# Kernel optimization log

Measured on AMD Instinct MI355X. Metric: run time of the kernel, lower is better.

Reference implementation:

```python
import jax, jax.numpy as jnp
import numpy as np

HIDDEN = 64
NUM_LAYERS = 6
BN_EPS = 1e-5


def setup_inputs() -> dict:
    key = jax.random.key(0)
    N, M = 1024, 1024
    num_nodes = N + M
    ks = jax.random.split(key, 12)
    x = jax.random.normal(ks[0], (num_nodes, 2), dtype=jnp.float32)
    # complete bipartite edges: (a, N+b) for all a in [0,N), b in [0,M), row-major so view(N,M) is meaningful
    row = jnp.repeat(jnp.arange(N, dtype=jnp.int64), M)
    col = N + jnp.tile(jnp.arange(M, dtype=jnp.int64), N)
    edge_index = jnp.stack([row, col], axis=0)
    s = 1.0 / np.sqrt(HIDDEN)
    return {
        "x": x,
        "edge_index": edge_index,
        "in_w": jax.random.normal(ks[1], (2, HIDDEN), jnp.float32) * 0.5,
        "in_b": jnp.zeros((HIDDEN,), jnp.float32),
        "conv_w": jax.random.normal(ks[2], (NUM_LAYERS, HIDDEN, HIDDEN), jnp.float32) * s,
        "conv_b": jnp.zeros((NUM_LAYERS, HIDDEN), jnp.float32),
        "bn_gamma": jnp.ones((NUM_LAYERS, HIDDEN), jnp.float32),
        "bn_beta": jnp.zeros((NUM_LAYERS, HIDDEN), jnp.float32),
        "out_w": jax.random.normal(ks[3], (2 * HIDDEN, 1), jnp.float32) * s,
        "out_b": jnp.zeros((1,), jnp.float32),
        "N": N,
        "M": M,
    }


def reference(x, edge_index, in_w, in_b, conv_w, conv_b, bn_gamma, bn_beta, out_w, out_b, N, M):
    num_nodes = x.shape[0]
    # GCN normalization with added self-loops (PyG GCNConv defaults)
    loops = jnp.arange(num_nodes, dtype=edge_index.dtype)
    row = jnp.concatenate([edge_index[0], loops])
    col = jnp.concatenate([edge_index[1], loops])
    deg = jax.ops.segment_sum(jnp.ones_like(col, dtype=x.dtype), col, num_segments=num_nodes)
    dinv = jnp.where(deg > 0, jax.lax.rsqrt(deg), 0.0)
    norm = dinv[row] * dinv[col]  # [E+num_nodes]

    h = jax.nn.relu(x @ in_w + in_b)
    for i in range(NUM_LAYERS):
        h_res = h
        hw = h @ conv_w[i]
        agg = jax.ops.segment_sum(hw[row] * norm[:, None], col, num_segments=num_nodes)
        h = agg + conv_b[i]
        # BatchNorm1d in training mode: batch stats, biased variance
        mu = h.mean(axis=0)
        var = ((h - mu) ** 2).mean(axis=0)
        h = (h - mu) * jax.lax.rsqrt(var + BN_EPS) * bn_gamma[i] + bn_beta[i]
        h = jax.nn.relu(h)
        if i > 0 and i % 2 == 1:
            h = h + h_res

    ef = jnp.concatenate([h[edge_index[0]], h[edge_index[1]]], axis=1)  # [E, 2H]
    scores = (ef @ out_w + out_b)[:, 0]
    return scores.reshape(N, M)
```

## Files before the change

kernel.cpp:

```cpp
#include <hip/hip_runtime.h>


#define NBLK 64
#define TAG_BASE 0x5EED1A00u

__device__ __forceinline__ float relu_(float x) { return x > 0.f ? x : 0.f; }

#define AT_LOAD(p)    __hip_atomic_load((p), __ATOMIC_RELAXED, __HIP_MEMORY_SCOPE_AGENT)
#define AT_STORE(p,v) __hip_atomic_store((p), (v), __ATOMIC_RELAXED, __HIP_MEMORY_SCOPE_AGENT)

#define ST_STRIDE_ULL 8192
#define UV_OFF        98304

__device__ __forceinline__ float2 poll_slots(const unsigned long long* stL,
                                             int slot0, int lane, unsigned tagexp)
{
    const unsigned long long* base = stL + lane * 2;
    for (;;) {
        unsigned long long sv[16], qv[16];
#pragma unroll
        for (int j = 0; j < 16; j++) {
            const unsigned long long* p = base + (slot0 + j) * 128;
            sv[j] = AT_LOAD(p);
            qv[j] = AT_LOAD(p + 1);
        }
        bool ok = true;
#pragma unroll
        for (int j = 0; j < 16; j++)
            ok = ok && ((unsigned)(sv[j] >> 32) == tagexp)
                    && ((unsigned)(qv[j] >> 32) == tagexp);
        if (ok) {
            float S = 0.f, Q = 0.f;
#pragma unroll
            for (int j = 0; j < 16; j++) {
                S += __uint_as_float((unsigned)sv[j]);
                Q += __uint_as_float((unsigned)qv[j]);
            }
            return make_float2(S, Q);
        }
        __builtin_amdgcn_s_sleep(1);
    }
}

__global__ __launch_bounds__(256, 1) void k_fused(
    const float* __restrict__ x,
    const float* __restrict__ in_w, const float* __restrict__ in_b,
    const float* __restrict__ conv_w,
    const float* __restrict__ bn_g, const float* __restrict__ bn_b,
    const float* __restrict__ out_w,
    unsigned int* __restrict__ ws)
{
    __shared__ float Wl[2][4096];
    __shared__ float hl[2048];
    __shared__ float Pp[3 * 2048];
    __shared__ float2 pstat[4][64];
    __shared__ float pcoef[64], scoef[64];
    __shared__ float g_lds[384], b_lds[384];
    __shared__ float ow_lds[128];

    const int t = threadIdx.x, b = blockIdx.x;
    const int w    = t >> 6;
    const int lane = t & 63;
    const int fi   = lane & 7;
    const int f0   = fi * 8;
    const int ng   = lane >> 3;
    const int n0   = ng * 4;
    const int sw   = ng & 3;
    const int kb   = w * 16;
    const bool isA = b < 32;
    unsigned long long* stu = (unsigned long long*)ws;
    float* uv = (float*)ws + UV_OFF;

    {
        const float4* src = (const float4*)conv_w;
        float4* dst = (float4*)Wl[0];
        dst[t]       = src[t];
        dst[t + 256] = src[t + 256];
        dst[t + 512] = src[t + 512];
        dst[t + 768] = src[t + 768];
        for (int i = t; i < 384; i += 256) { g_lds[i] = bn_g[i]; b_lds[i] = bn_b[i]; }
        if (t < 128) ow_lds[t] = out_w[t];
    }

    {
        const int nl = t >> 3, fj = (t & 7) * 8;
        const int rsw = (nl >> 2) & 3;
        const int node = b * 32 + nl;
        float x0 = x[node * 2], x1 = x[node * 2 + 1];
#pragma unroll
        for (int j = 0; j < 8; j++) {
            int f = fj + j;
            float v = relu_(fmaf(x0, in_w[f], fmaf(x1, in_w[64 + f], in_b[f])));
            hl[nl * 64 + ((((f >> 2)) ^ rsw) << 2) + (f & 3)] = v;
        }
    }
    __syncthreads();

    for (int layer = 0; layer < 6; layer++) {
        const float* Wb = Wl[layer & 1];
        float acc[4][8];
#pragma unroll
        for (int n = 0; n < 4; n++)
#pragma unroll
            for (int j = 0; j < 8; j++) acc[n][j] = 0.f;

#pragma unroll
        for (int kk = 0; kk < 16; kk += 4) {
            const int cb = (kb + kk) >> 2;
            float hv[4][4];
#pragma unroll
            for (int n = 0; n < 4; n++) {
                float4 h4 = *(const float4*)&hl[(n0 + n) * 64 + ((cb ^ sw) << 2)];
                hv[n][0] = h4.x; hv[n][1] = h4.y; hv[n][2] = h4.z; hv[n][3] = h4.w;
            }
#pragma unroll
            for (int j = 0; j < 4; j++) {
                const float* wr = Wb + (kb + kk + j) * 64 + f0;
                float4 w0 = *(const float4*)wr;
                float4 w1 = *(const float4*)(wr + 4);
                float wv[8] = {w0.x, w0.y, w0.z, w0.w, w1.x, w1.y, w1.z, w1.w};
#pragma unroll
                for (int n = 0; n < 4; n++)
#pragma unroll
                    for (int q = 0; q < 8; q++)
                        acc[n][q] = fmaf(hv[n][j], wv[q], acc[n][q]);
            }
        }

        float4 pf[6];
        const int idx = (w - 1) * 64 + lane;
        if (w > 0) {
            if (layer < 5) {
                const float4* src = (const float4*)(conv_w + (layer + 1) * 4096);
#pragma unroll
                for (int r = 0; r < 5; r++) pf[r] = src[idx + 192 * r];
                if (idx < 64) pf[5] = src[idx + 960];
            }
            float* Pw = Pp + (w - 1) * 2048;
#pragma unroll
            for (int n = 0; n < 4; n++) {
                float* prow = Pw + (n0 + n) * 64;
                *(float4*)&prow[((2 * fi)     ^ sw) << 2] =
                    make_float4(acc[n][0], acc[n][1], acc[n][2], acc[n][3]);
                *(float4*)&prow[((2 * fi + 1) ^ sw) << 2] =
                    make_float4(acc[n][4], acc[n][5], acc[n][6], acc[n][7]);
            }
        }
        __syncthreads();

        const unsigned tagexp = TAG_BASE + (unsigned)layer;
        unsigned long long* stL = stu + layer * ST_STRIDE_ULL;

        if (w == 0) {
#pragma unroll
            for (int r = 0; r < 3; r++) {
                const float* Pr = Pp + r * 2048;
#pragma unroll
                for (int n = 0; n < 4; n++) {
                    const float* prow = Pr + (n0 + n) * 64;
                    float4 p0 = *(const float4*)&prow[((2 * fi)     ^ sw) << 2];
                    float4 p1 = *(const float4*)&prow[((2 * fi + 1) ^ sw) << 2];
                    acc[n][0] += p0.x; acc[n][1] += p0.y; acc[n][2] += p0.z; acc[n][3] += p0.w;
                    acc[n][4] += p1.x; acc[n][5] += p1.y; acc[n][6] += p1.z; acc[n][7] += p1.w;
                }
            }
            float sv[8], qv[8];
#pragma unroll
            for (int j = 0; j < 8; j++) {
                sv[j] = (acc[0][j] + acc[1][j]) + (acc[2][j] + acc[3][j]);
                qv[j] = fmaf(acc[0][j], acc[0][j], fmaf(acc[1][j], acc[1][j],
                        fmaf(acc[2][j], acc[2][j], acc[3][j] * acc[3][j])));
            }
#pragma unroll
            for (int m = 8; m < 64; m <<= 1) {
#pragma unroll
                for (int j = 0; j < 8; j++) {
                    sv[j] += __shfl_xor(sv[j], m);
                    qv[j] += __shfl_xor(qv[j], m);
                }
            }
            {
                unsigned long long spack = ((unsigned long long)tagexp << 32)
                                         | (unsigned long long)__float_as_uint(sv[ng]);
                unsigned long long qpack = ((unsigned long long)tagexp << 32)
                                         | (unsigned long long)__float_as_uint(qv[ng]);
                unsigned long long* p = stL + b * 128 + (fi * 8 + ng) * 2;
                AT_STORE(p, spack);
                AT_STORE(p + 1, qpack);
            }
        }

        {
            float2 myp = poll_slots(stL, w * 16, lane, tagexp);
            pstat[w][lane] = myp;
        }
        __syncthreads();

        if (w > 0) {
            if (layer < 5) {
                float4* dst = (float4*)Wl[(layer + 1) & 1];
#pragma unroll
                for (int r = 0; r < 5; r++) dst[idx + 192 * r] = pf[r];
                if (idx < 64) dst[idx + 960] = pf[5];
            }
        } else {
            float2 a0 = pstat[0][lane], a1 = pstat[1][lane];
            float2 b0 = pstat[2][lane], b1 = pstat[3][lane];
            float SA = a0.x + a1.x, QA = a0.y + a1.y;
            float SB = b0.x + b1.x, QB = b0.y + b1.y;
            {
                const float c1 = 9.75609756097561e-4f;
                const float c2 = 3.1234752377721214e-2f;
                float sumAgg = SA + c1 * SB + 1024.f * c2 * SA;
                float sumSq  = QA + c1 * c1 * QB + 2.f * c1 * c2 * SA * SB
                             + 1024.f * c2 * c2 * SA * SA;
                float meanAgg = sumAgg * (1.f / 2048.f);
                float var = sumSq * (1.f / 2048.f) - meanAgg * meanAgg;
                float rstd = rsqrtf(var + 1e-5f);
                float scale = rstd * g_lds[layer * 64 + lane];
                float bt = b_lds[layer * 64 + lane];
                if (isA) { pcoef[lane] = scale;      scoef[lane] = bt - meanAgg * scale; }
                else     { pcoef[lane] = c1 * scale; scoef[lane] = bt + (c2 * SA - meanAgg) * scale; }
            }
            float pc[8], sc[8];
            {
                float4 p0 = *(const float4*)&pcoef[f0];
                float4 p1 = *(const float4*)&pcoef[f0 + 4];
                float4 s0 = *(const float4*)&scoef[f0];
                float4 s1 = *(const float4*)&scoef[f0 + 4];
                pc[0] = p0.x; pc[1] = p0.y; pc[2] = p0.z; pc[3] = p0.w;
                pc[4] = p1.x; pc[5] = p1.y; pc[6] = p1.z; pc[7] = p1.w;
                sc[0] = s0.x; sc[1] = s0.y; sc[2] = s0.z; sc[3] = s0.w;
                sc[4] = s1.x; sc[5] = s1.y; sc[6] = s1.z; sc[7] = s1.w;
            }

            float vals[4][8];
#pragma unroll
            for (int n = 0; n < 4; n++)
#pragma unroll
                for (int j = 0; j < 8; j++)
                    vals[n][j] = relu_(fmaf(acc[n][j], pc[j], sc[j]));
            if (layer == 1 || layer == 3 || layer == 5) {
#pragma unroll
                for (int n = 0; n < 4; n++) {
                    const float* hrow = hl + (n0 + n) * 64;
                    float4 r0 = *(const float4*)&hrow[((2 * fi)     ^ sw) << 2];
                    float4 r1 = *(const float4*)&hrow[((2 * fi + 1) ^ sw) << 2];
                    vals[n][0] += r0.x; vals[n][1] += r0.y; vals[n][2] += r0.z; vals[n][3] += r0.w;
                    vals[n][4] += r1.x; vals[n][5] += r1.y; vals[n][6] += r1.z; vals[n][7] += r1.w;
                }
            }
            if (layer < 5) {
#pragma unroll
                for (int n = 0; n < 4; n++) {
                    float* hrow = hl + (n0 + n) * 64;
                    *(float4*)&hrow[((2 * fi)     ^ sw) << 2] =
                        make_float4(vals[n][0], vals[n][1], vals[n][2], vals[n][3]);
                    *(float4*)&hrow[((2 * fi + 1) ^ sw) << 2] =
                        make_float4(vals[n][4], vals[n][5], vals[n][6], vals[n][7]);
                }
            } else {
                const float* wv = ow_lds + (isA ? 0 : 64) + f0;
                float4 o0 = *(const float4*)wv;
                float4 o1 = *(const float4*)(wv + 4);
                float d[4];
#pragma unroll
                for (int n = 0; n < 4; n++) {
                    d[n] = fmaf(vals[n][0], o0.x, fmaf(vals[n][1], o0.y,
                           fmaf(vals[n][2], o0.z, fmaf(vals[n][3], o0.w,
                           fmaf(vals[n][4], o1.x, fmaf(vals[n][5], o1.y,
                           fmaf(vals[n][6], o1.z, vals[n][7] * o1.w)))))));
                    d[n] += __shfl_xor(d[n], 1);
                    d[n] += __shfl_xor(d[n], 2);
                    d[n] += __shfl_xor(d[n], 4);
                }
                if (fi == 0) {
#pragma unroll
                    for (int n = 0; n < 4; n++)
                        AT_STORE((unsigned*)(uv + b * 32 + n0 + n),
                                 __float_as_uint(d[n]));
                }
            }
        }
        __syncthreads();
    }
}

__global__ __launch_bounds__(256) void k_out(const float* __restrict__ uv,
                                             const float* __restrict__ out_b,
                                             float* __restrict__ out) {
    const int a = blockIdx.x;
    const int t = threadIdx.x;
    float ua = uv[a] + out_b[0];
    float4 vv = ((const float4*)(uv + 1024))[t];
    ((float4*)(out + a * 1024))[t] =
        make_float4(ua + vv.x, ua + vv.y, ua + vv.z, ua + vv.w);
}

extern "C" void kernel_launch(void* const* d_in, const int* in_sizes, int n_in,
                              void* d_out, int out_size, void* d_ws, size_t ws_size,
                              hipStream_t stream) {
    const float* x      = (const float*)d_in[0];
    const float* in_w   = (const float*)d_in[2];
    const float* in_b   = (const float*)d_in[3];
    const float* conv_w = (const float*)d_in[4];
    const float* bn_g   = (const float*)d_in[6];
    const float* bn_b   = (const float*)d_in[7];
    const float* out_w  = (const float*)d_in[8];
    const float* out_b  = (const float*)d_in[9];
    float* out = (float*)d_out;

    unsigned int* ws = (unsigned int*)d_ws;
    const float* uv = (const float*)ws + UV_OFF;

    k_fused<<<NBLK, 256, 0, stream>>>(x, in_w, in_b, conv_w, bn_g, bn_b,
                                      out_w, ws);
    k_out<<<1024, 256, 0, stream>>>(uv, out_b, out);
}
```

Measured before the change: 116.2 us.

## Fuse output broadcast into persistent kernel using tagged flag-polled u/v values

Removes the separate k_out launch. Each block now publishes its per-node output projection as a tagged 64-bit word, then polls until all u/v values carry the tag and writes 16 rows of the N×M score matrix itself. This saves a kernel launch and its gap at the cost of a grid-wide spin wait at the end of the fused kernel. Only 64 blocks do the output write instead of 1024, which may reduce write bandwidth.

```diff
diff --git a/kernel.cpp b/kernel.cpp
--- a/kernel.cpp
+++ b/kernel.cpp
@@ -3,6 +3,7 @@
 
 #define NBLK 64
 #define TAG_BASE 0x5EED1A00u
+#define TAG_UV   (TAG_BASE + 6u)
 
 __device__ __forceinline__ float relu_(float x) { return x > 0.f ? x : 0.f; }
 
@@ -10,7 +11,7 @@
 #define AT_STORE(p,v) __hip_atomic_store((p), (v), __ATOMIC_RELAXED, __HIP_MEMORY_SCOPE_AGENT)
 
 #define ST_STRIDE_ULL 8192
-#define UV_OFF        98304
+#define UVT_OFF_ULL   49152
 
 __device__ __forceinline__ float2 poll_slots(const unsigned long long* stL,
                                              int slot0, int lane, unsigned tagexp)
@@ -47,7 +48,8 @@
     const float* __restrict__ in_w, const float* __restrict__ in_b,
     const float* __restrict__ conv_w,
     const float* __restrict__ bn_g, const float* __restrict__ bn_b,
-    const float* __restrict__ out_w,
+    const float* __restrict__ out_w, const float* __restrict__ out_b,
+    float* __restrict__ out,
     unsigned int* __restrict__ ws)
 {
     __shared__ float Wl[2][4096];
@@ -69,7 +71,7 @@
     const int kb   = w * 16;
     const bool isA = b < 32;
     unsigned long long* stu = (unsigned long long*)ws;
-    float* uv = (float*)ws + UV_OFF;
+    unsigned long long* uvt = stu + UVT_OFF_ULL;
 
     {
         const float4* src = (const float4*)conv_w;
@@ -276,25 +278,46 @@
                 }
                 if (fi == 0) {
 #pragma unroll
-                    for (int n = 0; n < 4; n++)
-                        AT_STORE((unsigned*)(uv + b * 32 + n0 + n),
-                                 __float_as_uint(d[n]));
+                    for (int n = 0; n < 4; n++) {
+                        unsigned long long pk = ((unsigned long long)TAG_UV << 32)
+                                              | (unsigned long long)__float_as_uint(d[n]);
+                        AT_STORE(uvt + b * 32 + n0 + n, pk);
+                    }
                 }
             }
         }
         __syncthreads();
     }
-}
-
-__global__ __launch_bounds__(256) void k_out(const float* __restrict__ uv,
-                                             const float* __restrict__ out_b,
-                                             float* __restrict__ out) {
-    const int a = blockIdx.x;
-    const int t = threadIdx.x;
-    float ua = uv[a] + out_b[0];
-    float4 vv = ((const float4*)(uv + 1024))[t];
-    ((float4*)(out + a * 1024))[t] =
-        make_float4(ua + vv.x, ua + vv.y, ua + vv.z, ua + vv.w);
+
+    {
+        const float ob = out_b[0];
+        unsigned long long vw[4], uw[16];
+        for (;;) {
+            bool ok = true;
+#pragma unroll
+            for (int j = 0; j < 4; j++) vw[j] = AT_LOAD(uvt + 1024 + t * 4 + j);
+#pragma unroll
+            for (int r = 0; r < 16; r++) uw[r] = AT_LOAD(uvt + b * 16 + r);
+#pragma unroll
+            for (int j = 0; j < 4; j++)
+                ok = ok && ((unsigned)(vw[j] >> 32) == TAG_UV);
+#pragma unroll
+            for (int r = 0; r < 16; r++)
+                ok = ok && ((unsigned)(uw[r] >> 32) == TAG_UV);
+            if (ok) break;
+            __builtin_amdgcn_s_sleep(2);
+        }
+        float v0 = __uint_as_float((unsigned)vw[0]);
+        float v1 = __uint_as_float((unsigned)vw[1]);
+        float v2 = __uint_as_float((unsigned)vw[2]);
+        float v3 = __uint_as_float((unsigned)vw[3]);
+#pragma unroll
+        for (int r = 0; r < 16; r++) {
+            float ua = __uint_as_float((unsigned)uw[r]) + ob;
+            ((float4*)(out + (b * 16 + r) * 1024))[t] =
+                make_float4(ua + v0, ua + v1, ua + v2, ua + v3);
+        }
+    }
 }
 
 extern "C" void kernel_launch(void* const* d_in, const int* in_sizes, int n_in,
@@ -309,11 +332,8 @@
     const float* out_w  = (const float*)d_in[8];
     const float* out_b  = (const float*)d_in[9];
     float* out = (float*)d_out;
-
     unsigned int* ws = (unsigned int*)d_ws;
-    const float* uv = (const float*)ws + UV_OFF;
 
     k_fused<<<NBLK, 256, 0, stream>>>(x, in_w, in_b, conv_w, bn_g, bn_b,
-                                      out_w, ws);
-    k_out<<<1024, 256, 0, stream>>>(uv, out_b, out);
+                                      out_w, out_b, out, ws);
 }
```

Measured after the change: 118.9 us. +2.3%, slower.
